# Kernel optimization log

Measured on AMD Instinct MI355X. Metric: run time of the kernel, lower is better.

The kernel has to match this reference:

```python
import jax, jax.numpy as jnp
import numpy as np

B, D, H, W = 8, 768, 32, 32
C, K = 2, 8
COORD_DIM = 128
GRID = 16
DIST_THRESH = 5
NUM_STEPS = 3
STEP_SIZE = 0.1
HW = H * W


def _pair_indices():
    # Static grid of sampled points (stride = max(1, H//grid_size)) and all
    # ordered pairs with Manhattan distance in (0, 5] -- mirrors the torch loops.
    stride = max(1, H // GRID)
    pi, pj = np.meshgrid(np.arange(0, H, stride), np.arange(0, W, stride), indexing='ij')
    pi, pj = pi.ravel(), pj.ravel()
    d = np.abs(pi[:, None] - pi[None, :]) + np.abs(pj[:, None] - pj[None, :])
    a, b = np.nonzero((d > 0) & (d <= DIST_THRESH))
    return (pi[a] * W + pj[a]).astype(np.int32), (pi[b] * W + pj[b]).astype(np.int32)


def setup_inputs() -> dict:
    key = jax.random.key(0)
    ks = jax.random.split(key, 16)
    IN = 2 * D + COORD_DIM  # 1664

    def n(i, shape, s=1.0):
        return jax.random.normal(ks[i], shape, dtype=jnp.float32) * s

    return {
        'features': n(0, (B, D, H, W)),
        'cam_raw': jax.random.uniform(ks[1], (B, C, H, W), dtype=jnp.float32),
        'y_primary': jax.random.uniform(ks[2], (B, C), dtype=jnp.float32),
        'eps': n(3, (B, K)),
        'coord_emb': n(4, (256 * 256, COORD_DIM), 0.02),
        'aff_W1': n(5, (C, IN, 256), 0.02), 'aff_b1': jnp.zeros((C, 256), jnp.float32),
        'aff_W2': n(6, (C, 256, 128), 0.05), 'aff_b2': jnp.zeros((C, 128), jnp.float32),
        'aff_W3': n(7, (C, 128, 1), 0.05), 'aff_b3': jnp.zeros((C, 1), jnp.float32),
        'mu_W1': n(8, (D, 256), 0.02), 'mu_b1': jnp.zeros((256,), jnp.float32),
        'mu_W2': n(9, (256, K), 0.05), 'mu_b2': jnp.zeros((K,), jnp.float32),
        'ls_W1': n(10, (D, 256), 0.02), 'ls_b1': jnp.zeros((256,), jnp.float32),
        'ls_W2': n(11, (256, K), 0.05), 'ls_b2': jnp.zeros((K,), jnp.float32),
        'conf_scale': jnp.array(1.0, jnp.float32),
        'conf_bias': jnp.array(0.0, jnp.float32),
    }


def reference(features, cam_raw, y_primary, eps, coord_emb,
              aff_W1, aff_b1, aff_W2, aff_b2, aff_W3, aff_b3,
              mu_W1, mu_b1, mu_W2, mu_b2, ls_W1, ls_b1, ls_W2, ls_b2,
              conf_scale, conf_bias):
    idx_a_np, idx_b_np = _pair_indices()
    idx_a, idx_b = jnp.asarray(idx_a_np), jnp.asarray(idx_b_np)
    P = idx_a.shape[0]

    # --- SubClassPosterior on globally pooled features ---
    f_global = features.mean(axis=(2, 3))                      # (B, D)
    z_mu = jax.nn.relu(f_global @ mu_W1 + mu_b1) @ mu_W2 + mu_b2
    z_logstd = jax.nn.relu(f_global @ ls_W1 + ls_b1) @ ls_W2 + ls_b2
    z_samples = z_mu + jnp.exp(z_logstd) * eps

    # --- ClassConditionalAffinity: batched gather + grouped MLP over all pairs ---
    feat = features.reshape(B, D, HW)
    f1 = feat[:, :, idx_a].transpose(0, 2, 1)                  # (B, P, D)
    f2 = feat[:, :, idx_b].transpose(0, 2, 1)                  # (B, P, D)
    ce = 0.5 * (coord_emb[idx_a] + coord_emb[idx_b])           # (P, E)
    x = jnp.concatenate([f1, f2, jnp.broadcast_to(ce, (B, P, COORD_DIM))], axis=-1)
    h = jax.nn.relu(jnp.einsum('bpi,cio->bcpo', x, aff_W1) + aff_b1[:, None, :])
    h = jax.nn.relu(jnp.einsum('bcpi,cio->bcpo', h, aff_W2) + aff_b2[:, None, :])
    logit = (jnp.einsum('bcpi,cio->bcpo', h, aff_W3) + aff_b3[:, None, :])[..., 0]
    val = jax.nn.sigmoid(logit)                                # (B, C, P)

    # A = where(mask, sigmoid(mlp), I); pairs are strictly off-diagonal & unique
    A = jnp.broadcast_to(jnp.eye(HW, dtype=features.dtype), (B, C, HW, HW))
    A = A.at[:, :, idx_a, idx_b].set(val)
    A = A / (A.sum(axis=3, keepdims=True) + 1e-8)              # row-normalize

    # --- AnisotropicDiffusion: M <- M + dt * (A M - deg * M) ---
    M = cam_raw.reshape(B, C, HW)
    deg = A.sum(axis=3)                                        # (B, C, HW)
    for _ in range(NUM_STEPS):
        L = jnp.einsum('bcij,bcj->bci', A, M) - deg * M
        M = M + STEP_SIZE * L
    cam_refined = jnp.clip(M.reshape(B, C, H, W), 0.0, 1.0)

    confidence = jax.nn.sigmoid(conf_scale * cam_refined + conf_bias)
    return cam_refined, z_mu, z_logstd, z_samples, A, confidence
```

## Files before the change

kernel.cpp:

```cpp
#include <hip/hip_runtime.h>
#include <math.h>

#define BB 8
#define DD 768
#define HWN 1024
#define NS 256
#define PPAD 3072
#define O1 256
#define O2 128

typedef __attribute__((ext_vector_type(8))) short bf16x8;
typedef __attribute__((ext_vector_type(4))) float f32x4;

__constant__ int c_du[12] = {1,-1,0,0,2,-2,0,0,1, 1,-1,-1};
__constant__ int c_dv[12] = {0, 0,1,-1,0, 0,2,-2,1,-1, 1,-1};
__constant__ signed char c_rk[25] = {
  -1,-1, 5,-1,-1,
  -1,11, 1,10,-1,
   7, 3,-1, 2, 6,
  -1, 9, 0, 8,-1,
  -1,-1, 4,-1,-1};

__device__ inline ushort f2bf(float x) {
  unsigned u = __float_as_uint(x);
  u += 0x7FFF + ((u >> 16) & 1);
  return (ushort)(u >> 16);
}
__device__ inline float bf2f(ushort h) { return __uint_as_float(((unsigned)h) << 16); }

__global__ void __launch_bounds__(256) k_pool(const float* __restrict__ feat,
                                              float* __restrict__ fg,
                                              ushort* __restrict__ g16) {
  int row = blockIdx.x;
  int t = threadIdx.x;
  const float4 v = reinterpret_cast<const float4*>(feat + (size_t)row * HWN)[t];
  float s = v.x + v.y + v.z + v.w;
#pragma unroll
  for (int m = 32; m >= 1; m >>= 1) s += __shfl_xor(s, m, 64);
  __shared__ float red[4];
  if ((t & 63) == 0) red[t >> 6] = s;
  if ((t & 8) == 0) {
    int b = row / DD, d = row - b * DD;
    int u = t >> 4, r = t & 7;
    int s1 = u * 16 + 2 * r;
    g16[((size_t)(b * NS + s1)) * DD + d] = f2bf(v.x);
    g16[((size_t)(b * NS + s1 + 1)) * DD + d] = f2bf(v.z);
  }
  __syncthreads();
  if (t == 0) fg[row] = (red[0] + red[1] + red[2] + red[3]) * (1.0f / 1024.0f);
}

__global__ void __launch_bounds__(256) k_zpart(const float* __restrict__ fg,
    const float* __restrict__ muW1, const float* __restrict__ lsW1,
    float* __restrict__ zscr) {
  int chunk = blockIdx.x, path = blockIdx.y, b = blockIdx.z;
  int t = threadIdx.x;
  int rg = t >> 6, ct = t & 63;
  __shared__ float sf[128];
  __shared__ __align__(16) float red[4][256];
  if (t < 128) sf[t] = fg[b * DD + chunk * 128 + t];
  __syncthreads();
  const float* W = (path ? lsW1 : muW1) + (size_t)(chunk * 128) * 256;
  float acc[4] = {0.f, 0.f, 0.f, 0.f};
#pragma unroll 4
  for (int it = 0; it < 32; it++) {
    int d = it * 4 + rg;
    float f = sf[d];
    float4 w = *reinterpret_cast<const float4*>(W + (size_t)d * 256 + ct * 4);
    acc[0] = fmaf(f, w.x, acc[0]);
    acc[1] = fmaf(f, w.y, acc[1]);
    acc[2] = fmaf(f, w.z, acc[2]);
    acc[3] = fmaf(f, w.w, acc[3]);
  }
  *reinterpret_cast<float4*>(&red[rg][ct * 4]) =
      make_float4(acc[0], acc[1], acc[2], acc[3]);
  __syncthreads();
  zscr[(((size_t)(b * 2 + path)) * 6 + chunk) * 256 + t] =
      red[0][t] + red[1][t] + red[2][t] + red[3][t];
}

__global__ void __launch_bounds__(256) k_zfinish(const float* __restrict__ zscr,
    const float* __restrict__ mub1, const float* __restrict__ muW2,
    const float* __restrict__ mub2,
    const float* __restrict__ lsb1, const float* __restrict__ lsW2,
    const float* __restrict__ lsb2,
    const float* __restrict__ eps,
    float* __restrict__ o_zmu, float* __restrict__ o_zls, float* __restrict__ o_zs) {
  int b = blockIdx.x;
  int t = threadIdx.x;
  __shared__ float shm[256], shl[256];
  __shared__ float zres[2][8];
  float hm = mub1[t], hl = lsb1[t];
#pragma unroll
  for (int ch = 0; ch < 6; ch++) {
    hm += zscr[(((size_t)(b * 2 + 0)) * 6 + ch) * 256 + t];
    hl += zscr[(((size_t)(b * 2 + 1)) * 6 + ch) * 256 + t];
  }
  shm[t] = fmaxf(hm, 0.f);
  shl[t] = fmaxf(hl, 0.f);
  __syncthreads();
  if (t < 128 && (t & 63) < 8) {
    int path = t >> 6, kk = t & 7;
    const float* W2 = path ? lsW2 : muW2;
    const float* bi = path ? lsb2 : mub2;
    const float* sh = path ? shl : shm;
    float z = bi[kk];
    for (int i = 0; i < 256; i++) z = fmaf(sh[i], W2[i * 8 + kk], z);
    zres[path][kk] = z;
  }
  __syncthreads();
  if (t < 8) {
    float zm = zres[0][t], zl = zres[1][t];
    o_zmu[b * 8 + t] = zm;
    o_zls[b * 8 + t] = zl;
    o_zs[b * 8 + t] = zm + expf(zl) * eps[b * 8 + t];
  }
}

__global__ void __launch_bounds__(256) k_EH(const float* __restrict__ cemb,
                                            const float* __restrict__ W1,
                                            const float* __restrict__ b1,
                                            float* __restrict__ EH) {
  int bs = blockIdx.x;
  int c = bs >> 8, s = bs & 255;
  int u = s >> 4, v = s & 15;
  int pix = (u << 6) + (v << 1);
  __shared__ float ce[128];
  int t = threadIdx.x;
  if (t < 128) ce[t] = cemb[(size_t)pix * 128 + t];
  __syncthreads();
  const float* W = W1 + ((size_t)c * 1664 + 1536) * O1;
  float acc = 0.f;
  for (int e = 0; e < 128; e++) acc = fmaf(ce[e], W[(size_t)e * O1 + t], acc);
  EH[((size_t)(c * NS + s)) * O1 + t] = 0.5f * (acc + b1[c * O1 + t]);
}

__global__ void __launch_bounds__(256) k_transpose(const float* __restrict__ W1,
    const float* __restrict__ W2, ushort* __restrict__ WT16, ushort* __restrict__ W2T16) {
  int blk = blockIdx.x, t = threadIdx.x;
  const float* src; ushort* dst; int K, N, k0, n0;
  if (blk < 192) {
    int ch = blk / 48, r = blk % 48;
    int c = ch & 1, half = ch >> 1;
    src = W1 + ((size_t)c * 1664 + half * 768) * 256;
    dst = WT16 + (size_t)ch * 256 * 768;
    K = 768; N = 256; k0 = (r >> 2) * 64; n0 = (r & 3) * 64;
  } else {
    int r = blk - 192;
    int c = r >> 3; int q = r & 7;
    src = W2 + (size_t)c * 256 * 128;
    dst = W2T16 + (size_t)c * 128 * 256;
    K = 256; N = 128; k0 = (q >> 1) * 64; n0 = (q & 1) * 64;
  }
  __shared__ float T[64][65];
  for (int i = 0; i < 16; i++) {
    int idx = i * 256 + t; int kl = idx >> 6, nl = idx & 63;
    T[kl][nl] = src[(size_t)(k0 + kl) * N + n0 + nl];
  }
  __syncthreads();
  for (int i = 0; i < 16; i++) {
    int idx = i * 256 + t; int nl = idx >> 6, kl = idx & 63;
    dst[(size_t)(n0 + nl) * K + k0 + kl] = f2bf(T[kl][nl]);
  }
}

__global__ void __launch_bounds__(256) k_gemm_mfma(const ushort* __restrict__ g16,
    const ushort* __restrict__ WT16, const float* __restrict__ EHb,
    ushort* __restrict__ Fb16) {
  int mt = blockIdx.x, nt = blockIdx.y, ch = blockIdx.z;
  int c = ch & 1;
  int row0 = mt * 64, col0 = nt * 64;
  int t = threadIdx.x;
  int wid = t >> 6, l = t & 63;
  int wm = wid & 1, wn = wid >> 1;
  int lm = l & 15, lk = (l >> 4) * 8;
  __shared__ float ehs[64][64];
  int s0 = row0 & 255;
  for (int i = 0; i < 16; i++) {
    int idx = i * 256 + t; int rl = idx >> 6, nl = idx & 63;
    ehs[rl][nl] = EHb[((size_t)(c * 256 + s0 + rl)) * 256 + col0 + nl];
  }
  f32x4 acc[2][2] = {};
  const ushort* ap0 = g16 + (size_t)(row0 + wm * 32 + lm) * DD + lk;
  const ushort* bp0 = WT16 + ((size_t)ch * 256 + col0 + wn * 32 + lm) * DD + lk;
#pragma unroll 4
  for (int k0 = 0; k0 < DD; k0 += 32) {
    bf16x8 a0 = *(const bf16x8*)(ap0 + k0);
    bf16x8 a1 = *(const bf16x8*)(ap0 + 16 * DD + k0);
    bf16x8 b0 = *(const bf16x8*)(bp0 + k0);
    bf16x8 b1 = *(const bf16x8*)(bp0 + 16 * DD + k0);
    acc[0][0] = __builtin_amdgcn_mfma_f32_16x16x32_bf16(a0, b0, acc[0][0], 0, 0, 0);
    acc[0][1] = __builtin_amdgcn_mfma_f32_16x16x32_bf16(a0, b1, acc[0][1], 0, 0, 0);
    acc[1][0] = __builtin_amdgcn_mfma_f32_16x16x32_bf16(a1, b0, acc[1][0], 0, 0, 0);
    acc[1][1] = __builtin_amdgcn_mfma_f32_16x16x32_bf16(a1, b1, acc[1][1], 0, 0, 0);
  }
  __syncthreads();
#pragma unroll
  for (int i = 0; i < 2; i++)
#pragma unroll
    for (int jj = 0; jj < 2; jj++)
#pragma unroll
      for (int r = 0; r < 4; r++) {
        int rm = wm * 32 + i * 16 + (l >> 4) * 4 + r;
        int cn = wn * 32 + jj * 16 + lm;
        float vo = acc[i][jj][r] + ehs[rm][cn];
        Fb16[((size_t)ch * 2048 + row0 + rm) * 256 + col0 + cn] = f2bf(vo);
      }
}

__global__ void __launch_bounds__(256) k_pairmlp_mfma(const ushort* __restrict__ Fb16,
    const ushort* __restrict__ W2T16, const float* __restrict__ b2,
    const float* __restrict__ W3, const float* __restrict__ b3,
    float* __restrict__ val) {
  int blk = blockIdx.x;
  int bc = blk / 48, grp = blk - bc * 48;
  int b = bc >> 1, c = bc & 1;
  int t = threadIdx.x;
  int wid = t >> 6, l = t & 63;
  int wm = wid & 1, wn = wid >> 1;
  int lm = l & 15, lk = (l >> 4) * 8;
  __shared__ ushort h1s[64 * 256];
  __shared__ float psum[2][64];
  {
    int p_l = t >> 2, q = t & 3;
    int j = grp * 64 + p_l;
    int s = j / 12, ko = j - s * 12;
    int u = s >> 4, v = s & 15;
    int ub = u + c_du[ko], vb = v + c_dv[ko];
    bool vld = (ub >= 0) && (ub < 16) && (vb >= 0) && (vb < 16);
    int sb = vld ? ub * 16 + vb : s;
    const ushort* f1p = Fb16 + ((size_t)(c * 2048 + b * 256 + s)) * 256 + q * 64;
    const ushort* f2p = Fb16 + ((size_t)((2 + c) * 2048 + b * 256 + sb)) * 256 + q * 64;
    char* hb = (char*)h1s;
#pragma unroll
    for (int kk = 0; kk < 64; kk += 8) {
      bf16x8 x1 = *(const bf16x8*)(f1p + kk);
      bf16x8 x2 = *(const bf16x8*)(f2p + kk);
      bf16x8 o;
#pragma unroll
      for (int e = 0; e < 8; e++) {
        float a = bf2f((ushort)x1[e]) + bf2f((ushort)x2[e]);
        o[e] = (short)f2bf(fmaxf(a, 0.f));
      }
      int byt = (p_l * 512 + (q * 64 + kk) * 2) ^ ((p_l & 7) << 4);
      *(bf16x8*)(hb + byt) = o;
    }
  }
  __syncthreads();
  f32x4 acc[2][4] = {};
  const ushort* wp = W2T16 + ((size_t)(c * 128 + wn * 64 + lm)) * 256 + lk;
  const char* hb = (const char*)h1s;
  int p0 = wm * 32 + lm;
  int swz = (p0 & 7) << 4;
#pragma unroll 2
  for (int k0 = 0; k0 < 256; k0 += 32) {
    bf16x8 a0 = *(const bf16x8*)(hb + ((p0 * 512 + (k0 + lk) * 2) ^ swz));
    bf16x8 a1 = *(const bf16x8*)(hb + (((p0 + 16) * 512 + (k0 + lk) * 2) ^ swz));
#pragma unroll
    for (int nf = 0; nf < 4; nf++) {
      bf16x8 bb = *(const bf16x8*)(wp + nf * 16 * 256 + k0);
      acc[0][nf] = __builtin_amdgcn_mfma_f32_16x16x32_bf16(a0, bb, acc[0][nf], 0, 0, 0);
      acc[1][nf] = __builtin_amdgcn_mfma_f32_16x16x32_bf16(a1, bb, acc[1][nf], 0, 0, 0);
    }
  }
  float b2v[4], w3v[4];
#pragma unroll
  for (int nf = 0; nf < 4; nf++) {
    int col = wn * 64 + nf * 16 + lm;
    b2v[nf] = b2[c * 128 + col];
    w3v[nf] = W3[c * 128 + col];
  }
  float part[2][4];
#pragma unroll
  for (int mf = 0; mf < 2; mf++)
#pragma unroll
    for (int r = 0; r < 4; r++) {
      float ssum = 0.f;
#pragma unroll
      for (int nf = 0; nf < 4; nf++) {
        float h = fmaxf(acc[mf][nf][r] + b2v[nf], 0.f);
        ssum = fmaf(h, w3v[nf], ssum);
      }
      part[mf][r] = ssum;
    }
#pragma unroll
  for (int m = 1; m <= 8; m <<= 1)
#pragma unroll
    for (int mf = 0; mf < 2; mf++)
#pragma unroll
      for (int r = 0; r < 4; r++)
        part[mf][r] += __shfl_xor(part[mf][r], m, 64);
  if (lm == 0) {
#pragma unroll
    for (int mf = 0; mf < 2; mf++)
#pragma unroll
      for (int r = 0; r < 4; r++)
        psum[wn][wm * 32 + mf * 16 + (l >> 4) * 4 + r] = part[mf][r];
  }
  __syncthreads();
  if (t < 64) {
    int jj = grp * 64 + t;
    int ss = jj / 12, kk2 = jj - ss * 12;
    int uu = ss >> 4, vv2 = ss & 15;
    int ub2 = uu + c_du[kk2], vb2 = vv2 + c_dv[kk2];
    bool vld = (ub2 >= 0) && (ub2 < 16) && (vb2 >= 0) && (vb2 < 16);
    float lg = psum[0][t] + psum[1][t] + b3[c];
    float sv = 1.0f / (1.0f + expf(-lg));
    val[(size_t)bc * PPAD + jj] = vld ? sv : 0.0f;
  }
}

__global__ void __launch_bounds__(256) k_writeA(const float* __restrict__ val,
                                                float* __restrict__ A) {
  int blk = blockIdx.x;
  int bc = blk >> 10, row = blk & 1023;
  int t = threadIdx.x;
  size_t base = (size_t)bc * HWN * HWN + (size_t)row * HWN;
  int pi = row >> 5, pj = row & 31;
  float4 o = make_float4(0.f, 0.f, 0.f, 0.f);
  if (((pi | pj) & 1) == 0) {
    int u = pi >> 1, v = pj >> 1;
    int s = u * 16 + v;
    __shared__ float sv[12];
    __shared__ float sInv;
    if (t < 12) sv[t] = val[(size_t)bc * PPAD + s * 12 + t];
    __syncthreads();
    if (t == 0) {
      float ssum = 1.f;
      for (int k = 0; k < 12; k++) ssum += sv[k];
      sInv = 1.f / (ssum + 1e-8f);
    }
    __syncthreads();
    float inv = sInv;
    float vo[4];
#pragma unroll
    for (int e = 0; e < 4; e++) {
      int col = t * 4 + e;
      float x = 0.f;
      if (col == row) {
        x = inv;
      } else if ((col & 33) == 0) {
        int cu = col >> 6, cv = (col & 31) >> 1;
        int du = cu - u + 2, dv = cv - v + 2;
        if (((unsigned)du < 5u) && ((unsigned)dv < 5u)) {
          int k = c_rk[du * 5 + dv];
          if (k >= 0) x = sv[k] * inv;
        }
      }
      vo[e] = x;
    }
    o = make_float4(vo[0], vo[1], vo[2], vo[3]);
  } else {
    if ((row >> 2) == t) {
      float dv = 1.0f / (1.0f + 1e-8f);
      int e = row & 3;
      if (e == 0) o.x = dv; else if (e == 1) o.y = dv;
      else if (e == 2) o.z = dv; else o.w = dv;
    }
  }
  reinterpret_cast<float4*>(A + base)[t] = o;
}

__global__ void __launch_bounds__(256) k_diffuse(const float* __restrict__ cam,
    const float* __restrict__ val,
    const float* __restrict__ csc, const float* __restrict__ cbi,
    float* __restrict__ o_cam, float* __restrict__ o_conf) {
  int bc = blockIdx.x;
  int t = threadIdx.x;
  __shared__ float M[NS];
  int u = t >> 4, v = t & 15;
  int pix = (u << 6) + (v << 1);
  const float* camr = cam + (size_t)bc * HWN;
  float m = camr[pix];
  float vv[12];
  int nb[12];
  float ssum = 1.f;
#pragma unroll
  for (int k = 0; k < 12; k++) {
    int ub = u + c_du[k], vb = v + c_dv[k];
    bool vld = (ub >= 0) && (ub < 16) && (vb >= 0) && (vb < 16);
    nb[k] = vld ? ub * 16 + vb : t;
    vv[k] = vld ? val[(size_t)bc * PPAD + t * 12 + k] : 0.0f;
    ssum += vv[k];
  }
  float inv = 1.0f / (ssum + 1e-8f);
  float degn = ssum * inv;
  M[t] = m;
  __syncthreads();
  for (int step = 0; step < 3; step++) {
    float accv = m;
#pragma unroll
    for (int k = 0; k < 12; k++) accv = fmaf(vv[k], M[nb[k]], accv);
    float L = accv * inv - degn * m;
    m = fmaf(0.1f, L, m);
    __syncthreads();
    M[t] = m;
    __syncthreads();
  }
  float scale = csc[0], bias = cbi[0];
  for (int p = t; p < HWN; p += 256) {
    int ppi = p >> 5, ppj = p & 31;
    float x;
    if (((ppi | ppj) & 1) == 0) x = M[(ppi >> 1) * 16 + (ppj >> 1)];
    else x = camr[p];
    x = fminf(fmaxf(x, 0.0f), 1.0f);
    o_cam[(size_t)bc * HWN + p] = x;
    o_conf[(size_t)bc * HWN + p] = 1.0f / (1.0f + expf(-(scale * x + bias)));
  }
}

extern "C" void kernel_launch(void* const* d_in, const int* in_sizes, int n_in,
                              void* d_out, int out_size, void* d_ws, size_t ws_size,
                              hipStream_t stream) {
  const float* feat = (const float*)d_in[0];
  const float* cam  = (const float*)d_in[1];
  const float* eps  = (const float*)d_in[3];
  const float* cemb = (const float*)d_in[4];
  const float* aW1  = (const float*)d_in[5];
  const float* ab1  = (const float*)d_in[6];
  const float* aW2  = (const float*)d_in[7];
  const float* ab2  = (const float*)d_in[8];
  const float* aW3  = (const float*)d_in[9];
  const float* ab3  = (const float*)d_in[10];
  const float* muW1 = (const float*)d_in[11];
  const float* mub1 = (const float*)d_in[12];
  const float* muW2 = (const float*)d_in[13];
  const float* mub2 = (const float*)d_in[14];
  const float* lsW1 = (const float*)d_in[15];
  const float* lsb1 = (const float*)d_in[16];
  const float* lsW2 = (const float*)d_in[17];
  const float* lsb2 = (const float*)d_in[18];
  const float* csc  = (const float*)d_in[19];
  const float* cbi  = (const float*)d_in[20];

  float* out = (float*)d_out;
  float* o_cam  = out;
  float* o_zmu  = out + 16384;
  float* o_zls  = out + 16448;
  float* o_zs   = out + 16512;
  float* o_A    = out + 16576;
  float* o_conf = out + 16793792;

  float*  fg    = o_A;
  float*  EHb   = o_A + 6144;
  ushort* g16   = (ushort*)(o_A + 137216);
  ushort* WT16  = (ushort*)(o_A + 923648);
  ushort* W2T16 = (ushort*)(o_A + 1316864);
  ushort* Fb16  = (ushort*)(o_A + 1349632);
  float*  zscr  = o_A + 2398208;
  float*  valb  = (float*)d_ws;

  hipLaunchKernelGGL(k_pool, dim3(BB * DD), dim3(256), 0, stream, feat, fg, g16);
  hipLaunchKernelGGL(k_zpart, dim3(6, 2, BB), dim3(256), 0, stream, fg, muW1, lsW1, zscr);
  hipLaunchKernelGGL(k_zfinish, dim3(BB), dim3(256), 0, stream, zscr, mub1, muW2,
                     mub2, lsb1, lsW2, lsb2, eps, o_zmu, o_zls, o_zs);
  hipLaunchKernelGGL(k_EH, dim3(512), dim3(256), 0, stream, cemb, aW1, ab1, EHb);
  hipLaunchKernelGGL(k_transpose, dim3(208), dim3(256), 0, stream, aW1, aW2, WT16, W2T16);
  hipLaunchKernelGGL(k_gemm_mfma, dim3(32, 4, 4), dim3(256), 0, stream, g16, WT16, EHb, Fb16);
  hipLaunchKernelGGL(k_pairmlp_mfma, dim3(768), dim3(256), 0, stream, Fb16, W2T16,
                     ab2, aW3, ab3, valb);
  hipLaunchKernelGGL(k_writeA, dim3(16384), dim3(256), 0, stream, valb, o_A);
  hipLaunchKernelGGL(k_diffuse, dim3(16), dim3(256), 0, stream, cam, valb,
                     csc, cbi, o_cam, o_conf);
}
```

Before: 98.69 us.

## Merge independent kernels into four block-range-dispatched launches

Combines pooling, coordinate-embedding projection and weight transposes into one pre-kernel. It also pairs the GEMM with the z-posterior partials, the pair MLP with the z finish, and the A write with the diffusion, each routed by block index. The goal is to remove launch overhead and inter-kernel gaps from the nine-launch chain, since independent pieces can now run concurrently. Shared memory per block becomes the maximum across the merged branches, which may reduce occupancy for the lighter branches.

```diff
diff --git a/kernel.cpp b/kernel.cpp
--- a/kernel.cpp
+++ b/kernel.cpp
@@ -28,384 +28,380 @@
 }
 __device__ inline float bf2f(ushort h) { return __uint_as_float(((unsigned)h) << 16); }
 
-__global__ void __launch_bounds__(256) k_pool(const float* __restrict__ feat,
-                                              float* __restrict__ fg,
-                                              ushort* __restrict__ g16) {
-  int row = blockIdx.x;
+__global__ void __launch_bounds__(256) k_pre(const float* __restrict__ feat,
+    const float* __restrict__ cemb, const float* __restrict__ W1,
+    const float* __restrict__ b1, const float* __restrict__ W2,
+    float* __restrict__ fg, ushort* __restrict__ g16,
+    float* __restrict__ EH, ushort* __restrict__ WT16, ushort* __restrict__ W2T16) {
+  __shared__ __align__(16) float sm[64 * 65];
+  int blk = blockIdx.x;
   int t = threadIdx.x;
-  const float4 v = reinterpret_cast<const float4*>(feat + (size_t)row * HWN)[t];
-  float s = v.x + v.y + v.z + v.w;
-#pragma unroll
-  for (int m = 32; m >= 1; m >>= 1) s += __shfl_xor(s, m, 64);
-  __shared__ float red[4];
-  if ((t & 63) == 0) red[t >> 6] = s;
-  if ((t & 8) == 0) {
-    int b = row / DD, d = row - b * DD;
-    int u = t >> 4, r = t & 7;
-    int s1 = u * 16 + 2 * r;
-    g16[((size_t)(b * NS + s1)) * DD + d] = f2bf(v.x);
-    g16[((size_t)(b * NS + s1 + 1)) * DD + d] = f2bf(v.z);
+  if (blk < 6144) {
+    int row = blk;
+    const float4 v = reinterpret_cast<const float4*>(feat + (size_t)row * HWN)[t];
+    float s = v.x + v.y + v.z + v.w;
+#pragma unroll
+    for (int m = 32; m >= 1; m >>= 1) s += __shfl_xor(s, m, 64);
+    if ((t & 63) == 0) sm[t >> 6] = s;
+    if ((t & 8) == 0) {
+      int b = row / DD, d = row - b * DD;
+      int u = t >> 4, r = t & 7;
+      int s1 = u * 16 + 2 * r;
+      g16[((size_t)(b * NS + s1)) * DD + d] = f2bf(v.x);
+      g16[((size_t)(b * NS + s1 + 1)) * DD + d] = f2bf(v.z);
+    }
+    __syncthreads();
+    if (t == 0) fg[row] = (sm[0] + sm[1] + sm[2] + sm[3]) * (1.0f / 1024.0f);
+  } else if (blk < 6656) {
+    int bs = blk - 6144;
+    int c = bs >> 8, s = bs & 255;
+    int u = s >> 4, v = s & 15;
+    int pix = (u << 6) + (v << 1);
+    float* ce = sm;
+    if (t < 128) ce[t] = cemb[(size_t)pix * 128 + t];
+    __syncthreads();
+    const float* W = W1 + ((size_t)c * 1664 + 1536) * O1;
+    float acc = 0.f;
+    for (int e = 0; e < 128; e++) acc = fmaf(ce[e], W[(size_t)e * O1 + t], acc);
+    EH[((size_t)(c * NS + s)) * O1 + t] = 0.5f * (acc + b1[c * O1 + t]);
+  } else {
+    int r0 = blk - 6656;
+    const float* src; ushort* dst; int K, N, k0, n0;
+    if (r0 < 192) {
+      int ch = r0 / 48, r = r0 % 48;
+      int c = ch & 1, half = ch >> 1;
+      src = W1 + ((size_t)c * 1664 + half * 768) * 256;
+      dst = WT16 + (size_t)ch * 256 * 768;
+      K = 768; N = 256; k0 = (r >> 2) * 64; n0 = (r & 3) * 64;
+    } else {
+      int r = r0 - 192;
+      int c = r >> 3; int q = r & 7;
+      src = W2 + (size_t)c * 256 * 128;
+      dst = W2T16 + (size_t)c * 128 * 256;
+      K = 256; N = 128; k0 = (q >> 1) * 64; n0 = (q & 1) * 64;
+    }
+    float (*T)[65] = reinterpret_cast<float(*)[65]>(sm);
+    for (int i = 0; i < 16; i++) {
+      int idx = i * 256 + t; int kl = idx >> 6, nl = idx & 63;
+      T[kl][nl] = src[(size_t)(k0 + kl) * N + n0 + nl];
+    }
+    __syncthreads();
+    for (int i = 0; i < 16; i++) {
+      int idx = i * 256 + t; int nl = idx >> 6, kl = idx & 63;
+      dst[(size_t)(n0 + nl) * K + k0 + kl] = f2bf(T[kl][nl]);
+    }
   }
-  __syncthreads();
-  if (t == 0) fg[row] = (red[0] + red[1] + red[2] + red[3]) * (1.0f / 1024.0f);
-}
-
-__global__ void __launch_bounds__(256) k_zpart(const float* __restrict__ fg,
-    const float* __restrict__ muW1, const float* __restrict__ lsW1,
-    float* __restrict__ zscr) {
-  int chunk = blockIdx.x, path = blockIdx.y, b = blockIdx.z;
+}
+
+__global__ void __launch_bounds__(256) k_mid(const ushort* __restrict__ g16,
+    const ushort* __restrict__ WT16, const float* __restrict__ EHb,
+    const float* __restrict__ fg, const float* __restrict__ muW1,
+    const float* __restrict__ lsW1,
+    ushort* __restrict__ Fb16, float* __restrict__ zscr) {
+  __shared__ __align__(16) float sm[4096];
+  int blk = blockIdx.x;
   int t = threadIdx.x;
-  int rg = t >> 6, ct = t & 63;
-  __shared__ float sf[128];
-  __shared__ __align__(16) float red[4][256];
-  if (t < 128) sf[t] = fg[b * DD + chunk * 128 + t];
-  __syncthreads();
-  const float* W = (path ? lsW1 : muW1) + (size_t)(chunk * 128) * 256;
-  float acc[4] = {0.f, 0.f, 0.f, 0.f};
+  if (blk < 512) {
+    int mt = blk & 31, nt = (blk >> 5) & 3, ch = blk >> 7;
+    int c = ch & 1;
+    int row0 = mt * 64, col0 = nt * 64;
+    int wid = t >> 6, l = t & 63;
+    int wm = wid & 1, wn = wid >> 1;
+    int lm = l & 15, lk = (l >> 4) * 8;
+    float (*ehs)[64] = reinterpret_cast<float(*)[64]>(sm);
+    int s0 = row0 & 255;
+    for (int i = 0; i < 16; i++) {
+      int idx = i * 256 + t; int rl = idx >> 6, nl = idx & 63;
+      ehs[rl][nl] = EHb[((size_t)(c * 256 + s0 + rl)) * 256 + col0 + nl];
+    }
+    f32x4 acc[2][2] = {};
+    const ushort* ap0 = g16 + (size_t)(row0 + wm * 32 + lm) * DD + lk;
+    const ushort* bp0 = WT16 + ((size_t)ch * 256 + col0 + wn * 32 + lm) * DD + lk;
 #pragma unroll 4
-  for (int it = 0; it < 32; it++) {
-    int d = it * 4 + rg;
-    float f = sf[d];
-    float4 w = *reinterpret_cast<const float4*>(W + (size_t)d * 256 + ct * 4);
-    acc[0] = fmaf(f, w.x, acc[0]);
-    acc[1] = fmaf(f, w.y, acc[1]);
-    acc[2] = fmaf(f, w.z, acc[2]);
-    acc[3] = fmaf(f, w.w, acc[3]);
+    for (int k0 = 0; k0 < DD; k0 += 32) {
+      bf16x8 a0 = *(const bf16x8*)(ap0 + k0);
+      bf16x8 a1 = *(const bf16x8*)(ap0 + 16 * DD + k0);
+      bf16x8 b0 = *(const bf16x8*)(bp0 + k0);
+      bf16x8 b1 = *(const bf16x8*)(bp0 + 16 * DD + k0);
+      acc[0][0] = __builtin_amdgcn_mfma_f32_16x16x32_bf16(a0, b0, acc[0][0], 0, 0, 0);
+      acc[0][1] = __builtin_amdgcn_mfma_f32_16x16x32_bf16(a0, b1, acc[0][1], 0, 0, 0);
+      acc[1][0] = __builtin_amdgcn_mfma_f32_16x16x32_bf16(a1, b0, acc[1][0], 0, 0, 0);
+      acc[1][1] = __builtin_amdgcn_mfma_f32_16x16x32_bf16(a1, b1, acc[1][1], 0, 0, 0);
+    }
+    __syncthreads();
+#pragma unroll
+    for (int i = 0; i < 2; i++)
+#pragma unroll
+      for (int jj = 0; jj < 2; jj++)
+#pragma unroll
+        for (int r = 0; r < 4; r++) {
+          int rm = wm * 32 + i * 16 + (l >> 4) * 4 + r;
+          int cn = wn * 32 + jj * 16 + lm;
+          float vo = acc[i][jj][r] + ehs[rm][cn];
+          Fb16[((size_t)ch * 2048 + row0 + rm) * 256 + col0 + cn] = f2bf(vo);
+        }
+  } else {
+    int i = blk - 512;
+    int chunk = i % 6, path = (i / 6) & 1, b = i / 12;
+    int rg = t >> 6, ct = t & 63;
+    float* sf = sm;
+    float (*red)[256] = reinterpret_cast<float(*)[256]>(sm + 128);
+    if (t < 128) sf[t] = fg[b * DD + chunk * 128 + t];
+    __syncthreads();
+    const float* W = (path ? lsW1 : muW1) + (size_t)(chunk * 128) * 256;
+    float acc[4] = {0.f, 0.f, 0.f, 0.f};
+#pragma unroll 4
+    for (int it = 0; it < 32; it++) {
+      int d = it * 4 + rg;
+      float f = sf[d];
+      float4 w = *reinterpret_cast<const float4*>(W + (size_t)d * 256 + ct * 4);
+      acc[0] = fmaf(f, w.x, acc[0]);
+      acc[1] = fmaf(f, w.y, acc[1]);
+      acc[2] = fmaf(f, w.z, acc[2]);
+      acc[3] = fmaf(f, w.w, acc[3]);
+    }
+    *reinterpret_cast<float4*>(&red[rg][ct * 4]) =
+        make_float4(acc[0], acc[1], acc[2], acc[3]);
+    __syncthreads();
+    zscr[(((size_t)(b * 2 + path)) * 6 + chunk) * 256 + t] =
+        red[0][t] + red[1][t] + red[2][t] + red[3][t];
   }
-  *reinterpret_cast<float4*>(&red[rg][ct * 4]) =
-      make_float4(acc[0], acc[1], acc[2], acc[3]);
-  __syncthreads();
-  zscr[(((size_t)(b * 2 + path)) * 6 + chunk) * 256 + t] =
-      red[0][t] + red[1][t] + red[2][t] + red[3][t];
-}
-
-__global__ void __launch_bounds__(256) k_zfinish(const float* __restrict__ zscr,
+}
+
+__global__ void __launch_bounds__(256) k_pair(const ushort* __restrict__ Fb16,
+    const ushort* __restrict__ W2T16, const float* __restrict__ b2,
+    const float* __restrict__ W3, const float* __restrict__ b3,
+    const float* __restrict__ zscr,
     const float* __restrict__ mub1, const float* __restrict__ muW2,
     const float* __restrict__ mub2,
     const float* __restrict__ lsb1, const float* __restrict__ lsW2,
-    const float* __restrict__ lsb2,
-    const float* __restrict__ eps,
+    const float* __restrict__ lsb2, const float* __restrict__ eps,
+    float* __restrict__ val,
     float* __restrict__ o_zmu, float* __restrict__ o_zls, float* __restrict__ o_zs) {
-  int b = blockIdx.x;
+  __shared__ __align__(16) ushort h1s[64 * 256];
+  __shared__ float psum2[2][64];
+  int blk = blockIdx.x;
   int t = threadIdx.x;
-  __shared__ float shm[256], shl[256];
-  __shared__ float zres[2][8];
-  float hm = mub1[t], hl = lsb1[t];
-#pragma unroll
-  for (int ch = 0; ch < 6; ch++) {
-    hm += zscr[(((size_t)(b * 2 + 0)) * 6 + ch) * 256 + t];
-    hl += zscr[(((size_t)(b * 2 + 1)) * 6 + ch) * 256 + t];
+  if (blk < 768) {
+    int bc = blk / 48, grp = blk - bc * 48;
+    int b = bc >> 1, c = bc & 1;
+    int wid = t >> 6, l = t & 63;
+    int wm = wid & 1, wn = wid >> 1;
+    int lm = l & 15, lk = (l >> 4) * 8;
+    {
+      int p_l = t >> 2, q = t & 3;
+      int j = grp * 64 + p_l;
+      int s = j / 12, ko = j - s * 12;
+      int u = s >> 4, v = s & 15;
+      int ub = u + c_du[ko], vb = v + c_dv[ko];
+      bool vld = (ub >= 0) && (ub < 16) && (vb >= 0) && (vb < 16);
+      int sb = vld ? ub * 16 + vb : s;
+      const ushort* f1p = Fb16 + ((size_t)(c * 2048 + b * 256 + s)) * 256 + q * 64;
+      const ushort* f2p = Fb16 + ((size_t)((2 + c) * 2048 + b * 256 + sb)) * 256 + q * 64;
+      char* hb = (char*)h1s;
+#pragma unroll
+      for (int kk = 0; kk < 64; kk += 8) {
+        bf16x8 x1 = *(const bf16x8*)(f1p + kk);
+        bf16x8 x2 = *(const bf16x8*)(f2p + kk);
+        bf16x8 o;
+#pragma unroll
+        for (int e = 0; e < 8; e++) {
+          float a = bf2f((ushort)x1[e]) + bf2f((ushort)x2[e]);
+          o[e] = (short)f2bf(fmaxf(a, 0.f));
+        }
+        int byt = (p_l * 512 + (q * 64 + kk) * 2) ^ ((p_l & 7) << 4);
+        *(bf16x8*)(hb + byt) = o;
+      }
+    }
+    __syncthreads();
+    f32x4 acc[2][4] = {};
+    const ushort* wp = W2T16 + ((size_t)(c * 128 + wn * 64 + lm)) * 256 + lk;
+    const char* hb = (const char*)h1s;
+    int p0 = wm * 32 + lm;
+    int swz = (p0 & 7) << 4;
+#pragma unroll 2
+    for (int k0 = 0; k0 < 256; k0 += 32) {
+      bf16x8 a0 = *(const bf16x8*)(hb + ((p0 * 512 + (k0 + lk) * 2) ^ swz));
+      bf16x8 a1 = *(const bf16x8*)(hb + (((p0 + 16) * 512 + (k0 + lk) * 2) ^ swz));
+#pragma unroll
+      for (int nf = 0; nf < 4; nf++) {
+        bf16x8 bb = *(const bf16x8*)(wp + nf * 16 * 256 + k0);
+        acc[0][nf] = __builtin_amdgcn_mfma_f32_16x16x32_bf16(a0, bb, acc[0][nf], 0, 0, 0);
+        acc[1][nf] = __builtin_amdgcn_mfma_f32_16x16x32_bf16(a1, bb, acc[1][nf], 0, 0, 0);
+      }
+    }
+    float b2v[4], w3v[4];
+#pragma unroll
+    for (int nf = 0; nf < 4; nf++) {
+      int col = wn * 64 + nf * 16 + lm;
+      b2v[nf] = b2[c * 128 + col];
+      w3v[nf] = W3[c * 128 + col];
+    }
+    float part[2][4];
+#pragma unroll
+    for (int mf = 0; mf < 2; mf++)
+#pragma unroll
+      for (int r = 0; r < 4; r++) {
+        float ssum = 0.f;
+#pragma unroll
+        for (int nf = 0; nf < 4; nf++) {
+          float h = fmaxf(acc[mf][nf][r] + b2v[nf], 0.f);
+          ssum = fmaf(h, w3v[nf], ssum);
+        }
+        part[mf][r] = ssum;
+      }
+#pragma unroll
+    for (int m = 1; m <= 8; m <<= 1)
+#pragma unroll
+      for (int mf = 0; mf < 2; mf++)
+#pragma unroll
+        for (int r = 0; r < 4; r++)
+          part[mf][r] += __shfl_xor(part[mf][r], m, 64);
+    if (lm == 0) {
+#pragma unroll
+      for (int mf = 0; mf < 2; mf++)
+#pragma unroll
+        for (int r = 0; r < 4; r++)
+          psum2[wn][wm * 32 + mf * 16 + (l >> 4) * 4 + r] = part[mf][r];
+    }
+    __syncthreads();
+    if (t < 64) {
+      int jj = grp * 64 + t;
+      int ss = jj / 12, kk2 = jj - ss * 12;
+      int uu = ss >> 4, vv2 = ss & 15;
+      int ub2 = uu + c_du[kk2], vb2 = vv2 + c_dv[kk2];
+      bool vld = (ub2 >= 0) && (ub2 < 16) && (vb2 >= 0) && (vb2 < 16);
+      float lg = psum2[0][t] + psum2[1][t] + b3[c];
+      float sv = 1.0f / (1.0f + expf(-lg));
+      val[(size_t)bc * PPAD + jj] = vld ? sv : 0.0f;
+    }
+  } else {
+    int b = blk - 768;
+    float* shm = (float*)h1s;
+    float* shl = shm + 256;
+    float* zres = shm + 512;
+    float hm = mub1[t], hl = lsb1[t];
+#pragma unroll
+    for (int ch = 0; ch < 6; ch++) {
+      hm += zscr[(((size_t)(b * 2 + 0)) * 6 + ch) * 256 + t];
+      hl += zscr[(((size_t)(b * 2 + 1)) * 6 + ch) * 256 + t];
+    }
+    shm[t] = fmaxf(hm, 0.f);
+    shl[t] = fmaxf(hl, 0.f);
+    __syncthreads();
+    if (t < 128 && (t & 63) < 8) {
+      int path = t >> 6, kk = t & 7;
+      const float* W2p = path ? lsW2 : muW2;
+      const float* bi = path ? lsb2 : mub2;
+      const float* sh = path ? shl : shm;
+      float z = bi[kk];
+      for (int i = 0; i < 256; i++) z = fmaf(sh[i], W2p[i * 8 + kk], z);
+      zres[path * 8 + kk] = z;
+    }
+    __syncthreads();
+    if (t < 8) {
+      float zm = zres[t], zl = zres[8 + t];
+      o_zmu[b * 8 + t] = zm;
+      o_zls[b * 8 + t] = zl;
+      o_zs[b * 8 + t] = zm + expf(zl) * eps[b * 8 + t];
+    }
   }
-  shm[t] = fmaxf(hm, 0.f);
-  shl[t] = fmaxf(hl, 0.f);
-  __syncthreads();
-  if (t < 128 && (t & 63) < 8) {
-    int path = t >> 6, kk = t & 7;
-    const float* W2 = path ? lsW2 : muW2;
-    const float* bi = path ? lsb2 : mub2;
-    const float* sh = path ? shl : shm;
-    float z = bi[kk];
-    for (int i = 0; i < 256; i++) z = fmaf(sh[i], W2[i * 8 + kk], z);
-    zres[path][kk] = z;
-  }
-  __syncthreads();
-  if (t < 8) {
-    float zm = zres[0][t], zl = zres[1][t];
-    o_zmu[b * 8 + t] = zm;
-    o_zls[b * 8 + t] = zl;
-    o_zs[b * 8 + t] = zm + expf(zl) * eps[b * 8 + t];
-  }
-}
-
-__global__ void __launch_bounds__(256) k_EH(const float* __restrict__ cemb,
-                                            const float* __restrict__ W1,
-                                            const float* __restrict__ b1,
-                                            float* __restrict__ EH) {
-  int bs = blockIdx.x;
-  int c = bs >> 8, s = bs & 255;
-  int u = s >> 4, v = s & 15;
-  int pix = (u << 6) + (v << 1);
-  __shared__ float ce[128];
+}
+
+__global__ void __launch_bounds__(256) k_final(const float* __restrict__ val,
+    const float* __restrict__ cam,
+    const float* __restrict__ csc, const float* __restrict__ cbi,
+    float* __restrict__ A, float* __restrict__ o_cam, float* __restrict__ o_conf) {
+  __shared__ float smf[260];
+  int blk = blockIdx.x;
   int t = threadIdx.x;
-  if (t < 128) ce[t] = cemb[(size_t)pix * 128 + t];
-  __syncthreads();
-  const float* W = W1 + ((size_t)c * 1664 + 1536) * O1;
-  float acc = 0.f;
-  for (int e = 0; e < 128; e++) acc = fmaf(ce[e], W[(size_t)e * O1 + t], acc);
-  EH[((size_t)(c * NS + s)) * O1 + t] = 0.5f * (acc + b1[c * O1 + t]);
-}
-
-__global__ void __launch_bounds__(256) k_transpose(const float* __restrict__ W1,
-    const float* __restrict__ W2, ushort* __restrict__ WT16, ushort* __restrict__ W2T16) {
-  int blk = blockIdx.x, t = threadIdx.x;
-  const float* src; ushort* dst; int K, N, k0, n0;
-  if (blk < 192) {
-    int ch = blk / 48, r = blk % 48;
-    int c = ch & 1, half = ch >> 1;
-    src = W1 + ((size_t)c * 1664 + half * 768) * 256;
-    dst = WT16 + (size_t)ch * 256 * 768;
-    K = 768; N = 256; k0 = (r >> 2) * 64; n0 = (r & 3) * 64;
+  if (blk < 16384) {
+    int bc = blk >> 10, row = blk & 1023;
+    size_t base = (size_t)bc * HWN * HWN + (size_t)row * HWN;
+    int pi = row >> 5, pj = row & 31;
+    float4 o = make_float4(0.f, 0.f, 0.f, 0.f);
+    if (((pi | pj) & 1) == 0) {
+      int u = pi >> 1, v = pj >> 1;
+      int s = u * 16 + v;
+      float* sv = smf;
+      if (t < 12) sv[t] = val[(size_t)bc * PPAD + s * 12 + t];
+      __syncthreads();
+      if (t == 0) {
+        float ssum = 1.f;
+        for (int k = 0; k < 12; k++) ssum += sv[k];
+        smf[12] = 1.f / (ssum + 1e-8f);
+      }
+      __syncthreads();
+      float inv = smf[12];
+      float vo[4];
+#pragma unroll
+      for (int e = 0; e < 4; e++) {
+        int col = t * 4 + e;
+        float x = 0.f;
+        if (col == row) {
+          x = inv;
+        } else if ((col & 33) == 0) {
+          int cu = col >> 6, cv = (col & 31) >> 1;
+          int du = cu - u + 2, dv = cv - v + 2;
+          if (((unsigned)du < 5u) && ((unsigned)dv < 5u)) {
+            int k = c_rk[du * 5 + dv];
+            if (k >= 0) x = sv[k] * inv;
+          }
+        }
+        vo[e] = x;
+      }
+      o = make_float4(vo[0], vo[1], vo[2], vo[3]);
+    } else {
+      if ((row >> 2) == t) {
+        float dv = 1.0f / (1.0f + 1e-8f);
+        int e = row & 3;
+        if (e == 0) o.x = dv; else if (e == 1) o.y = dv;
+        else if (e == 2) o.z = dv; else o.w = dv;
+      }
+    }
+    reinterpret_cast<float4*>(A + base)[t] = o;
   } else {
-    int r = blk - 192;
-    int c = r >> 3; int q = r & 7;
-    src = W2 + (size_t)c * 256 * 128;
-    dst = W2T16 + (size_t)c * 128 * 256;
-    K = 256; N = 128; k0 = (q >> 1) * 64; n0 = (q & 1) * 64;
-  }
-  __shared__ float T[64][65];
-  for (int i = 0; i < 16; i++) {
-    int idx = i * 256 + t; int kl = idx >> 6, nl = idx & 63;
-    T[kl][nl] = src[(size_t)(k0 + kl) * N + n0 + nl];
-  }
-  __syncthreads();
-  for (int i = 0; i < 16; i++) {
-    int idx = i * 256 + t; int nl = idx >> 6, kl = idx & 63;
-    dst[(size_t)(n0 + nl) * K + k0 + kl] = f2bf(T[kl][nl]);
-  }
-}
-
-__global__ void __launch_bounds__(256) k_gemm_mfma(const ushort* __restrict__ g16,
-    const ushort* __restrict__ WT16, const float* __restrict__ EHb,
-    ushort* __restrict__ Fb16) {
-  int mt = blockIdx.x, nt = blockIdx.y, ch = blockIdx.z;
-  int c = ch & 1;
-  int row0 = mt * 64, col0 = nt * 64;
-  int t = threadIdx.x;
-  int wid = t >> 6, l = t & 63;
-  int wm = wid & 1, wn = wid >> 1;
-  int lm = l & 15, lk = (l >> 4) * 8;
-  __shared__ float ehs[64][64];
-  int s0 = row0 & 255;
-  for (int i = 0; i < 16; i++) {
-    int idx = i * 256 + t; int rl = idx >> 6, nl = idx & 63;
-    ehs[rl][nl] = EHb[((size_t)(c * 256 + s0 + rl)) * 256 + col0 + nl];
-  }
-  f32x4 acc[2][2] = {};
-  const ushort* ap0 = g16 + (size_t)(row0 + wm * 32 + lm) * DD + lk;
-  const ushort* bp0 = WT16 + ((size_t)ch * 256 + col0 + wn * 32 + lm) * DD + lk;
-#pragma unroll 4
-  for (int k0 = 0; k0 < DD; k0 += 32) {
-    bf16x8 a0 = *(const bf16x8*)(ap0 + k0);
-    bf16x8 a1 = *(const bf16x8*)(ap0 + 16 * DD + k0);
-    bf16x8 b0 = *(const bf16x8*)(bp0 + k0);
-    bf16x8 b1 = *(const bf16x8*)(bp0 + 16 * DD + k0);
-    acc[0][0] = __builtin_amdgcn_mfma_f32_16x16x32_bf16(a0, b0, acc[0][0], 0, 0, 0);
-    acc[0][1] = __builtin_amdgcn_mfma_f32_16x16x32_bf16(a0, b1, acc[0][1], 0, 0, 0);
-    acc[1][0] = __builtin_amdgcn_mfma_f32_16x16x32_bf16(a1, b0, acc[1][0], 0, 0, 0);
-    acc[1][1] = __builtin_amdgcn_mfma_f32_16x16x32_bf16(a1, b1, acc[1][1], 0, 0, 0);
-  }
-  __syncthreads();
-#pragma unroll
-  for (int i = 0; i < 2; i++)
-#pragma unroll
-    for (int jj = 0; jj < 2; jj++)
-#pragma unroll
-      for (int r = 0; r < 4; r++) {
-        int rm = wm * 32 + i * 16 + (l >> 4) * 4 + r;
-        int cn = wn * 32 + jj * 16 + lm;
-        float vo = acc[i][jj][r] + ehs[rm][cn];
-        Fb16[((size_t)ch * 2048 + row0 + rm) * 256 + col0 + cn] = f2bf(vo);
-      }
-}
-
-__global__ void __launch_bounds__(256) k_pairmlp_mfma(const ushort* __restrict__ Fb16,
-    const ushort* __restrict__ W2T16, const float* __restrict__ b2,
-    const float* __restrict__ W3, const float* __restrict__ b3,
-    float* __restrict__ val) {
-  int blk = blockIdx.x;
-  int bc = blk / 48, grp = blk - bc * 48;
-  int b = bc >> 1, c = bc & 1;
-  int t = threadIdx.x;
-  int wid = t >> 6, l = t & 63;
-  int wm = wid & 1, wn = wid >> 1;
-  int lm = l & 15, lk = (l >> 4) * 8;
-  __shared__ ushort h1s[64 * 256];
-  __shared__ float psum[2][64];
-  {
-    int p_l = t >> 2, q = t & 3;
-    int j = grp * 64 + p_l;
-    int s = j / 12, ko = j - s * 12;
-    int u = s >> 4, v = s & 15;
-    int ub = u + c_du[ko], vb = v + c_dv[ko];
-    bool vld = (ub >= 0) && (ub < 16) && (vb >= 0) && (vb < 16);
-    int sb = vld ? ub * 16 + vb : s;
-    const ushort* f1p = Fb16 + ((size_t)(c * 2048 + b * 256 + s)) * 256 + q * 64;
-    const ushort* f2p = Fb16 + ((size_t)((2 + c) * 2048 + b * 256 + sb)) * 256 + q * 64;
-    char* hb = (char*)h1s;
-#pragma unroll
-    for (int kk = 0; kk < 64; kk += 8) {
-      bf16x8 x1 = *(const bf16x8*)(f1p + kk);
-      bf16x8 x2 = *(const bf16x8*)(f2p + kk);
-      bf16x8 o;
-#pragma unroll
-      for (int e = 0; e < 8; e++) {
-        float a = bf2f((ushort)x1[e]) + bf2f((ushort)x2[e]);
-        o[e] = (short)f2bf(fmaxf(a, 0.f));
-      }
-      int byt = (p_l * 512 + (q * 64 + kk) * 2) ^ ((p_l & 7) << 4);
-      *(bf16x8*)(hb + byt) = o;
-    }
-  }
-  __syncthreads();
-  f32x4 acc[2][4] = {};
-  const ushort* wp = W2T16 + ((size_t)(c * 128 + wn * 64 + lm)) * 256 + lk;
-  const char* hb = (const char*)h1s;
-  int p0 = wm * 32 + lm;
-  int swz = (p0 & 7) << 4;
-#pragma unroll 2
-  for (int k0 = 0; k0 < 256; k0 += 32) {
-    bf16x8 a0 = *(const bf16x8*)(hb + ((p0 * 512 + (k0 + lk) * 2) ^ swz));
-    bf16x8 a1 = *(const bf16x8*)(hb + (((p0 + 16) * 512 + (k0 + lk) * 2) ^ swz));
-#pragma unroll
-    for (int nf = 0; nf < 4; nf++) {
-      bf16x8 bb = *(const bf16x8*)(wp + nf * 16 * 256 + k0);
-      acc[0][nf] = __builtin_amdgcn_mfma_f32_16x16x32_bf16(a0, bb, acc[0][nf], 0, 0, 0);
-      acc[1][nf] = __builtin_amdgcn_mfma_f32_16x16x32_bf16(a1, bb, acc[1][nf], 0, 0, 0);
-    }
-  }
-  float b2v[4], w3v[4];
-#pragma unroll
-  for (int nf = 0; nf < 4; nf++) {
-    int col = wn * 64 + nf * 16 + lm;
-    b2v[nf] = b2[c * 128 + col];
-    w3v[nf] = W3[c * 128 + col];
-  }
-  float part[2][4];
-#pragma unroll
-  for (int mf = 0; mf < 2; mf++)
-#pragma unroll
-    for (int r = 0; r < 4; r++) {
-      float ssum = 0.f;
-#pragma unroll
-      for (int nf = 0; nf < 4; nf++) {
-        float h = fmaxf(acc[mf][nf][r] + b2v[nf], 0.f);
-        ssum = fmaf(h, w3v[nf], ssum);
-      }
-      part[mf][r] = ssum;
-    }
-#pragma unroll
-  for (int m = 1; m <= 8; m <<= 1)
-#pragma unroll
-    for (int mf = 0; mf < 2; mf++)
-#pragma unroll
-      for (int r = 0; r < 4; r++)
-        part[mf][r] += __shfl_xor(part[mf][r], m, 64);
-  if (lm == 0) {
-#pragma unroll
-    for (int mf = 0; mf < 2; mf++)
-#pragma unroll
-      for (int r = 0; r < 4; r++)
-        psum[wn][wm * 32 + mf * 16 + (l >> 4) * 4 + r] = part[mf][r];
-  }
-  __syncthreads();
-  if (t < 64) {
-    int jj = grp * 64 + t;
-    int ss = jj / 12, kk2 = jj - ss * 12;
-    int uu = ss >> 4, vv2 = ss & 15;
-    int ub2 = uu + c_du[kk2], vb2 = vv2 + c_dv[kk2];
-    bool vld = (ub2 >= 0) && (ub2 < 16) && (vb2 >= 0) && (vb2 < 16);
-    float lg = psum[0][t] + psum[1][t] + b3[c];
-    float sv = 1.0f / (1.0f + expf(-lg));
-    val[(size_t)bc * PPAD + jj] = vld ? sv : 0.0f;
-  }
-}
-
-__global__ void __launch_bounds__(256) k_writeA(const float* __restrict__ val,
-                                                float* __restrict__ A) {
-  int blk = blockIdx.x;
-  int bc = blk >> 10, row = blk & 1023;
-  int t = threadIdx.x;
-  size_t base = (size_t)bc * HWN * HWN + (size_t)row * HWN;
-  int pi = row >> 5, pj = row & 31;
-  float4 o = make_float4(0.f, 0.f, 0.f, 0.f);
-  if (((pi | pj) & 1) == 0) {
-    int u = pi >> 1, v = pj >> 1;
-    int s = u * 16 + v;
-    __shared__ float sv[12];
-    __shared__ float sInv;
-    if (t < 12) sv[t] = val[(size_t)bc * PPAD + s * 12 + t];
-    __syncthreads();
-    if (t == 0) {
-      float ssum = 1.f;
-      for (int k = 0; k < 12; k++) ssum += sv[k];
-      sInv = 1.f / (ssum + 1e-8f);
-    }
-    __syncthreads();
-    float inv = sInv;
-    float vo[4];
-#pragma unroll
-    for (int e = 0; e < 4; e++) {
-      int col = t * 4 + e;
-      float x = 0.f;
-      if (col == row) {
-        x = inv;
-      } else if ((col & 33) == 0) {
-        int cu = col >> 6, cv = (col & 31) >> 1;
-        int du = cu - u + 2, dv = cv - v + 2;
-        if (((unsigned)du < 5u) && ((unsigned)dv < 5u)) {
-          int k = c_rk[du * 5 + dv];
-          if (k >= 0) x = sv[k] * inv;
-        }
-      }
-      vo[e] = x;
-    }
-    o = make_float4(vo[0], vo[1], vo[2], vo[3]);
-  } else {
-    if ((row >> 2) == t) {
-      float dv = 1.0f / (1.0f + 1e-8f);
-      int e = row & 3;
-      if (e == 0) o.x = dv; else if (e == 1) o.y = dv;
-      else if (e == 2) o.z = dv; else o.w = dv;
-    }
-  }
-  reinterpret_cast<float4*>(A + base)[t] = o;
-}
-
-__global__ void __launch_bounds__(256) k_diffuse(const float* __restrict__ cam,
-    const float* __restrict__ val,
-    const float* __restrict__ csc, const float* __restrict__ cbi,
-    float* __restrict__ o_cam, float* __restrict__ o_conf) {
-  int bc = blockIdx.x;
-  int t = threadIdx.x;
-  __shared__ float M[NS];
-  int u = t >> 4, v = t & 15;
-  int pix = (u << 6) + (v << 1);
-  const float* camr = cam + (size_t)bc * HWN;
-  float m = camr[pix];
-  float vv[12];
-  int nb[12];
-  float ssum = 1.f;
-#pragma unroll
-  for (int k = 0; k < 12; k++) {
-    int ub = u + c_du[k], vb = v + c_dv[k];
-    bool vld = (ub >= 0) && (ub < 16) && (vb >= 0) && (vb < 16);
-    nb[k] = vld ? ub * 16 + vb : t;
-    vv[k] = vld ? val[(size_t)bc * PPAD + t * 12 + k] : 0.0f;
-    ssum += vv[k];
-  }
-  float inv = 1.0f / (ssum + 1e-8f);
-  float degn = ssum * inv;
-  M[t] = m;
-  __syncthreads();
-  for (int step = 0; step < 3; step++) {
-    float accv = m;
-#pragma unroll
-    for (int k = 0; k < 12; k++) accv = fmaf(vv[k], M[nb[k]], accv);
-    float L = accv * inv - degn * m;
-    m = fmaf(0.1f, L, m);
-    __syncthreads();
+    int bc = blk - 16384;
+    float* M = smf;
+    int u = t >> 4, v = t & 15;
+    int pix = (u << 6) + (v << 1);
+    const float* camr = cam + (size_t)bc * HWN;
+    float m = camr[pix];
+    float vv[12];
+    int nb[12];
+    float ssum = 1.f;
+#pragma unroll
+    for (int k = 0; k < 12; k++) {
+      int ub = u + c_du[k], vb = v + c_dv[k];
+      bool vld = (ub >= 0) && (ub < 16) && (vb >= 0) && (vb < 16);
+      nb[k] = vld ? ub * 16 + vb : t;
+      vv[k] = vld ? val[(size_t)bc * PPAD + t * 12 + k] : 0.0f;
+      ssum += vv[k];
+    }
+    float inv = 1.0f / (ssum + 1e-8f);
+    float degn = ssum * inv;
     M[t] = m;
     __syncthreads();
-  }
-  float scale = csc[0], bias = cbi[0];
-  for (int p = t; p < HWN; p += 256) {
-    int ppi = p >> 5, ppj = p & 31;
-    float x;
-    if (((ppi | ppj) & 1) == 0) x = M[(ppi >> 1) * 16 + (ppj >> 1)];
-    else x = camr[p];
-    x = fminf(fmaxf(x, 0.0f), 1.0f);
-    o_cam[(size_t)bc * HWN + p] = x;
-    o_conf[(size_t)bc * HWN + p] = 1.0f / (1.0f + expf(-(scale * x + bias)));
+    for (int step = 0; step < 3; step++) {
+      float accv = m;
+#pragma unroll
+      for (int k = 0; k < 12; k++) accv = fmaf(vv[k], M[nb[k]], accv);
+      float L = accv * inv - degn * m;
+      m = fmaf(0.1f, L, m);
+      __syncthreads();
+      M[t] = m;
+      __syncthreads();
+    }
+    float scale = csc[0], bias = cbi[0];
+    for (int p = t; p < HWN; p += 256) {
+      int ppi = p >> 5, ppj = p & 31;
+      float x;
+      if (((ppi | ppj) & 1) == 0) x = M[(ppi >> 1) * 16 + (ppj >> 1)];
+      else x = camr[p];
+      x = fminf(fmaxf(x, 0.0f), 1.0f);
+      o_cam[(size_t)bc * HWN + p] = x;
+      o_conf[(size_t)bc * HWN + p] = 1.0f / (1.0f + expf(-(scale * x + bias)));
+    }
   }
 }
 
@@ -450,16 +446,14 @@
   float*  zscr  = o_A + 2398208;
   float*  valb  = (float*)d_ws;
 
-  hipLaunchKernelGGL(k_pool, dim3(BB * DD), dim3(256), 0, stream, feat, fg, g16);
-  hipLaunchKernelGGL(k_zpart, dim3(6, 2, BB), dim3(256), 0, stream, fg, muW1, lsW1, zscr);
-  hipLaunchKernelGGL(k_zfinish, dim3(BB), dim3(256), 0, stream, zscr, mub1, muW2,
-                     mub2, lsb1, lsW2, lsb2, eps, o_zmu, o_zls, o_zs);
-  hipLaunchKernelGGL(k_EH, dim3(512), dim3(256), 0, stream, cemb, aW1, ab1, EHb);
-  hipLaunchKernelGGL(k_transpose, dim3(208), dim3(256), 0, stream, aW1, aW2, WT16, W2T16);
-  hipLaunchKernelGGL(k_gemm_mfma, dim3(32, 4, 4), dim3(256), 0, stream, g16, WT16, EHb, Fb16);
-  hipLaunchKernelGGL(k_pairmlp_mfma, dim3(768), dim3(256), 0, stream, Fb16, W2T16,
-                     ab2, aW3, ab3, valb);
-  hipLaunchKernelGGL(k_writeA, dim3(16384), dim3(256), 0, stream, valb, o_A);
-  hipLaunchKernelGGL(k_diffuse, dim3(16), dim3(256), 0, stream, cam, valb,
-                     csc, cbi, o_cam, o_conf);
-}
+  hipLaunchKernelGGL(k_pre, dim3(6864), dim3(256), 0, stream,
+                     feat, cemb, aW1, ab1, aW2, fg, g16, EHb, WT16, W2T16);
+  hipLaunchKernelGGL(k_mid, dim3(608), dim3(256), 0, stream,
+                     g16, WT16, EHb, fg, muW1, lsW1, Fb16, zscr);
+  hipLaunchKernelGGL(k_pair, dim3(776), dim3(256), 0, stream,
+                     Fb16, W2T16, ab2, aW3, ab3, zscr,
+                     mub1, muW2, mub2, lsb1, lsW2, lsb2, eps,
+                     valb, o_zmu, o_zls, o_zs);
+  hipLaunchKernelGGL(k_final, dim3(16400), dim3(256), 0, stream,
+                     valb, cam, csc, cbi, o_A, o_cam, o_conf);
+}
```

Result: faster. 85.08 us (-13.8%).
